# Kernel optimization log

Measured on AMD Instinct MI355X. Metric: run time of the kernel, lower is better.

Reference implementation:

```python
import jax, jax.numpy as jnp
import numpy as np

B, N, C, D = 8, 16384, 256, 32
EPS = 1e-6


def setup_inputs() -> dict:
    key = jax.random.key(0)
    ks = jax.random.split(key, 16)
    g = lambda k, shape, s=0.05: jax.random.normal(k, shape, dtype=jnp.float32) * s
    inp = {
        "x": g(ks[0], (B, N, C), 1.0),
        "y": g(ks[1], (B, N, C), 1.0),
        "Wq": g(ks[2], (D, C)), "bq": g(ks[3], (D,), 0.01),
        "Wk": g(ks[4], (D, C)), "bk": g(ks[5], (D,), 0.01),
        "Wv": g(ks[6], (C, C)), "bv": g(ks[7], (C,), 0.01),
        "Wqy": g(ks[8], (D, C)), "bqy": g(ks[9], (D,), 0.01),
        "Wky": g(ks[10], (D, C)), "bky": g(ks[11], (D,), 0.01),
        "Wvy": g(ks[12], (C, C)), "bvy": g(ks[13], (C,), 0.01),
        # gammas are nn.Parameter(torch.zeros(1)); random-init so outputs/grads are nontrivial
        "gamma": jnp.full((1,), 0.7, jnp.float32),
        "gamma_y": jnp.full((1,), 0.6, jnp.float32),
        "gamma_cx": jnp.full((1,), 0.5, jnp.float32),
        "gamma_cy": jnp.full((1,), 0.4, jnp.float32),
        "wx1": jnp.float32(0.5), "wx2": jnp.float32(0.5),
        "wy1": jnp.float32(0.5), "wy2": jnp.float32(0.5),
    }
    return inp


def _conv1x1(t, W, b):
    # t: [b,c,n]; 1x1 Conv2d == per-position linear
    return jnp.einsum('oc,bcn->bon', W, t) + b[None, :, None]


def _l2norm(t):
    # torch l2_norm: divide each spatial column by its channel-dim L2 norm
    return t / jnp.linalg.norm(t, axis=-2, keepdims=True)


def _branch(Qt, Ksum, mat, vsum, n):
    # Qt:[b,n,d]  Ksum:[b,d]  mat=K@V^T:[b,d,c]  vsum:[b,c]
    tailor = 1.0 / (n + jnp.einsum('bnd,bd->bn', Qt, Ksum))      # [b,n]
    msum = vsum[:, :, None] + jnp.einsum('bnd,bdc->bcn', Qt, mat)  # [b,c,n]
    return msum * tailor[:, None, :]


def reference(x, y, Wq, bq, Wk, bk, Wv, bv, Wqy, bqy, Wky, bky, Wvy, bvy,
              gamma, gamma_y, gamma_cx, gamma_cy, wx1, wx2, wy1, wy2):
    b, n, c = x.shape
    xb = jnp.transpose(x, (0, 2, 1))  # [b,c,n]
    yb = jnp.transpose(y, (0, 2, 1))
    Q = _l2norm(_conv1x1(xb, Wq, bq))      # [b,d,n]
    K = _l2norm(_conv1x1(xb, Wk, bk))
    V = _conv1x1(xb, Wv, bv)               # [b,c,n]
    Qy = _l2norm(_conv1x1(yb, Wqy, bqy))
    Ky = _l2norm(_conv1x1(yb, Wky, bky))
    Vy = _conv1x1(yb, Wvy, bvy)
    Qt = jnp.transpose(Q, (0, 2, 1))       # [b,n,d]
    Qyt = jnp.transpose(Qy, (0, 2, 1))
    Ksum = K.sum(-1) + EPS                 # [b,d]
    Kysum = Ky.sum(-1) + EPS
    vsum = V.sum(-1)                       # [b,c]
    vysum = Vy.sum(-1)
    mat = jnp.einsum('bdn,bcn->bdc', K, V)     # [b,d,c]
    maty = jnp.einsum('bdn,bcn->bdc', Ky, Vy)
    att = gamma * _branch(Qt, Ksum, mat, vsum, n)          # self x
    atty = gamma_y * _branch(Qyt, Kysum, maty, vysum, n)   # self y
    att_cx = gamma_cx * _branch(Qt, Kysum, maty, vsum, n)  # cross x<-y
    att_cy = gamma_cy * _branch(Qyt, Ksum, mat, vysum, n)  # cross y<-x
    fx = jnp.transpose(att * wx1 + att_cx * wx2, (0, 2, 1))  # [b,n,c]
    fy = jnp.transpose(atty * wy1 + att_cy * wy2, (0, 2, 1))
    return (fx, fy)
```

## Files before the change

kernel.cpp:

```cpp
#include <hip/hip_runtime.h>

#define BB 8
#define NN 16384
#define CC 256
#define DD 32
#define EPSF 1e-6f

#define QBUF_FLOATS (2ull*BB*NN*DD)
#define ACC_STRIDE 8480
#define ACC_OFF QBUF_FLOATS
#define ACC_FLOATS (16*ACC_STRIDE)
#define FIN_OFF (ACC_OFF + ACC_FLOATS)
#define FIN_STRIDE 8480
#define WBF_OFF (FIN_OFF + 16*FIN_STRIDE)

typedef __attribute__((ext_vector_type(8))) short bh8;
typedef __attribute__((ext_vector_type(4))) float f4;
typedef __attribute__((ext_vector_type(2))) unsigned int u32x2;

__device__ __forceinline__ unsigned int bfp(float f) {
    unsigned int u = __float_as_uint(f);
    return (u + 0x7FFFu + ((u >> 16) & 1u)) >> 16;
}
__device__ __forceinline__ float bf2f(unsigned int h) {
    return __uint_as_float(h << 16);
}

#define MFMA16 __builtin_amdgcn_mfma_f32_16x16x32_bf16

#define LBAR() do { \
    asm volatile("s_waitcnt lgkmcnt(0)" ::: "memory"); \
    __builtin_amdgcn_s_barrier(); \
    __builtin_amdgcn_sched_barrier(0); \
} while (0)

__global__ __launch_bounds__(256)
void k0_cvt(const float* __restrict__ Wk, const float* __restrict__ Wq,
            const float* __restrict__ Wky, const float* __restrict__ Wqy,
            unsigned short* __restrict__ wbf)
{
    int i = blockIdx.x * 256 + threadIdx.x;
    const float* p = (i < 8192) ? Wk : (i < 16384) ? Wq : (i < 24576) ? Wky : Wqy;
    wbf[i] = (unsigned short)bfp(p[i & 8191]);
}

__global__ __launch_bounds__(256, 3)
void k1_proj(const float* __restrict__ x, const float* __restrict__ y,
             const unsigned short* __restrict__ wbf,
             const float* __restrict__ bk, const float* __restrict__ bq,
             const float* __restrict__ bky, const float* __restrict__ bqy,
             unsigned short* __restrict__ qbuf16, float* __restrict__ acc,
             float* __restrict__ pbuf)
{
    const int b = blockIdx.y, s = blockIdx.z;
    const float* __restrict__ src = (s ? y : x) + (size_t)b * NN * CC;
    unsigned short* __restrict__ qb = qbuf16 + (size_t)(s*BB + b) * NN * DD;
    float* __restrict__ accsb = acc + (size_t)(s*BB + b) * ACC_STRIDE;
    float* __restrict__ pout = pbuf + ((size_t)((s*BB + b) * 64 + blockIdx.x)) * 8192;

    __shared__ unsigned short Xsub[2][8192];
    __shared__ unsigned short Ksb[1024];
    __shared__ float red[4][32];
    __shared__ float xred[4][256];

    const int tid = threadIdx.x;
    const int w = tid >> 6, lane = tid & 63;
    const int l15 = lane & 15, l4 = lane >> 4;
    const int oct = lane & 31;
    const int rower = tid >> 5;

    const unsigned short* __restrict__ wm =
        wbf + (size_t)(s * 2 + (w >> 1)) * 8192 + (size_t)(16 * (w & 1) + l15) * 256 + 8 * l4;
    bh8 wf[8];
    #pragma unroll
    for (int ks = 0; ks < 8; ++ks) wf[ks] = *(const bh8*)(wm + 32 * ks);
    const float* __restrict__ bp = (w < 2) ? (s ? bky : bk) : (s ? bqy : bq);
    const f4 bias4 = *(const f4*)(bp + 16 * (w & 1) + 4 * l4);

    const int hv = (rower >> 2) & 1;
    const int wbyte0 = (hv * 2048 + (oct >> 1) * 128 + (rower & 3) * 32 + (oct & 1) * 16) ^ (hv << 4);
    int ab[2];
    #pragma unroll
    for (int pt = 0; pt < 2; ++pt) {
        int aq = 4 * pt + (l15 >> 2);
        ab[pt] = ((aq * 2048 + (l15 & 3) * 32 + (l4 & 1) * 16) ^ ((aq & 1) << 4)) + (l4 >> 1) * 128;
    }
    const unsigned xb0 = (unsigned)(uintptr_t)&Xsub[0][0];
    const unsigned kbase = (unsigned)(uintptr_t)&Ksb[0];
    const unsigned btr_rel = (unsigned)(2 * l4 * 2048 + 4 * w * 128 + l15 * 8);
    const unsigned atr = kbase + (unsigned)(2 * l4 * 256 + l15 * 8);

    f4 g2[2][4];
    #pragma unroll
    for (int dt = 0; dt < 2; ++dt)
        #pragma unroll
        for (int ct = 0; ct < 4; ++ct) g2[dt][ct] = (f4){0.f, 0.f, 0.f, 0.f};
    float xs[8];
    #pragma unroll
    for (int j = 0; j < 8; ++j) xs[j] = 0.f;
    float kreg[4] = {0.f, 0.f, 0.f, 0.f};

    const float* __restrict__ gbase = src + (size_t)(blockIdx.x * 256 + rower) * CC + oct * 8;
    float4 va[4], vb[4];

    #pragma unroll
    for (int it = 0; it < 4; ++it) {
        const float* g = gbase + (size_t)(it * 8) * CC;
        va[it] = *(const float4*)g;
        vb[it] = *(const float4*)(g + 4);
    }

    for (int ch = 0; ch < 8; ++ch) {
        const int cur = ch & 1;
        char* xcur = (char*)&Xsub[cur][0];

        #pragma unroll
        for (int it = 0; it < 4; ++it) {
            float4 A = va[it], B = vb[it];
            xs[0] += A.x; xs[1] += A.y; xs[2] += A.z; xs[3] += A.w;
            xs[4] += B.x; xs[5] += B.y; xs[6] += B.z; xs[7] += B.w;
            uint4 pk;
            pk.x = bfp(A.x) | (bfp(A.y) << 16);
            pk.y = bfp(A.z) | (bfp(A.w) << 16);
            pk.z = bfp(B.x) | (bfp(B.y) << 16);
            pk.w = bfp(B.z) | (bfp(B.w) << 16);
            *(uint4*)(xcur + wbyte0 + it * 4096) = pk;
        }
        if (ch < 7) {
            const float* gn = gbase + (size_t)((ch + 1) * 32) * CC;
            #pragma unroll
            for (int it = 0; it < 4; ++it) {
                const float* g = gn + (size_t)(it * 8) * CC;
                va[it] = *(const float4*)g;
                vb[it] = *(const float4*)(g + 4);
            }
        }
        LBAR();

        f4 a1[2];
        #pragma unroll
        for (int pt = 0; pt < 2; ++pt) a1[pt] = bias4;
        #pragma unroll
        for (int ks = 0; ks < 8; ++ks) {
            #pragma unroll
            for (int pt = 0; pt < 2; ++pt) {
                bh8 xbv = *(const bh8*)(xcur + ab[pt] + ks * 256);
                a1[pt] = MFMA16(wf[ks], xbv, a1[pt], 0, 0, 0);
            }
        }

        #pragma unroll
        for (int pt = 0; pt < 2; ++pt) {
            float ssv = a1[pt][0]*a1[pt][0] + a1[pt][1]*a1[pt][1]
                      + a1[pt][2]*a1[pt][2] + a1[pt][3]*a1[pt][3];
            ssv += __shfl_xor(ssv, 16);
            ssv += __shfl_xor(ssv, 32);
            if (l4 == 0) red[w][16 * pt + l15] = ssv;
        }
        LBAR();

        if (w < 2) {
            #pragma unroll
            for (int pt = 0; pt < 2; ++pt) {
                int p = 16 * pt + l15;
                float n = rsqrtf(red[0][p] + red[1][p]);
                float k0 = a1[pt][0]*n, k1 = a1[pt][1]*n, k2 = a1[pt][2]*n, k3 = a1[pt][3]*n;
                kreg[0] += k0; kreg[1] += k1; kreg[2] += k2; kreg[3] += k3;
                unsigned lo = bfp(k0) | (bfp(k1) << 16);
                unsigned hi = bfp(k2) | (bfp(k3) << 16);
                *(uint2*)((char*)Ksb + (p >> 2) * 256 + (w & 1) * 128 + (p & 3) * 32 + 8 * l4)
                    = make_uint2(lo, hi);
            }
        } else {
            #pragma unroll
            for (int pt = 0; pt < 2; ++pt) {
                int p = 16 * pt + l15;
                float n = rsqrtf(red[2][p] + red[3][p]);
                unsigned lo = bfp(a1[pt][0]*n) | (bfp(a1[pt][1]*n) << 16);
                unsigned hi = bfp(a1[pt][2]*n) | (bfp(a1[pt][3]*n) << 16);
                *(uint2*)(qb + (size_t)(blockIdx.x*256 + ch*32 + p) * DD + 16 * (w & 1) + 4 * l4)
                    = make_uint2(lo, hi);
            }
        }
        LBAR();

        {
            const unsigned kb = xb0 + (unsigned)(cur * 16384) + btr_rel;
            u32x2 ta0, ta1, ta2, ta3, tb0, tb1, tb2, tb3, tb4, tb5, tb6, tb7;
            asm volatile("ds_read_b64_tr_b16 %0, %1" : "=v"(ta0) : "v"(atr));
            asm volatile("ds_read_b64_tr_b16 %0, %1" : "=v"(ta1) : "v"(atr + 256u));
            asm volatile("ds_read_b64_tr_b16 %0, %1" : "=v"(ta2) : "v"(atr + 128u));
            asm volatile("ds_read_b64_tr_b16 %0, %1" : "=v"(ta3) : "v"(atr + 384u));
            asm volatile("ds_read_b64_tr_b16 %0, %1" : "=v"(tb0) : "v"(kb));
            asm volatile("ds_read_b64_tr_b16 %0, %1" : "=v"(tb1) : "v"((kb + 2048u) ^ 16u));
            asm volatile("ds_read_b64_tr_b16 %0, %1" : "=v"(tb2) : "v"(kb + 128u));
            asm volatile("ds_read_b64_tr_b16 %0, %1" : "=v"(tb3) : "v"((kb + 2176u) ^ 16u));
            asm volatile("ds_read_b64_tr_b16 %0, %1" : "=v"(tb4) : "v"(kb + 256u));
            asm volatile("ds_read_b64_tr_b16 %0, %1" : "=v"(tb5) : "v"((kb + 2304u) ^ 16u));
            asm volatile("ds_read_b64_tr_b16 %0, %1" : "=v"(tb6) : "v"(kb + 384u));
            asm volatile("ds_read_b64_tr_b16 %0, %1" : "=v"(tb7) : "v"((kb + 2432u) ^ 16u));
            asm volatile("s_waitcnt lgkmcnt(8)" ::: "memory");
            __builtin_amdgcn_sched_barrier(0);
            union { unsigned u[4]; bh8 v; } A0, A1;
            A0.u[0] = ta0[0]; A0.u[1] = ta0[1]; A0.u[2] = ta1[0]; A0.u[3] = ta1[1];
            A1.u[0] = ta2[0]; A1.u[1] = ta2[1]; A1.u[2] = ta3[0]; A1.u[3] = ta3[1];
            asm volatile("s_waitcnt lgkmcnt(6)" ::: "memory");
            __builtin_amdgcn_sched_barrier(0);
            {
                union { unsigned u[4]; bh8 v; } Bc;
                Bc.u[0] = tb0[0]; Bc.u[1] = tb0[1]; Bc.u[2] = tb1[0]; Bc.u[3] = tb1[1];
                g2[0][0] = MFMA16(A0.v, Bc.v, g2[0][0], 0, 0, 0);
                g2[1][0] = MFMA16(A1.v, Bc.v, g2[1][0], 0, 0, 0);
            }
            asm volatile("s_waitcnt lgkmcnt(4)" ::: "memory");
            __builtin_amdgcn_sched_barrier(0);
            {
                union { unsigned u[4]; bh8 v; } Bc;
                Bc.u[0] = tb2[0]; Bc.u[1] = tb2[1]; Bc.u[2] = tb3[0]; Bc.u[3] = tb3[1];
                g2[0][1] = MFMA16(A0.v, Bc.v, g2[0][1], 0, 0, 0);
                g2[1][1] = MFMA16(A1.v, Bc.v, g2[1][1], 0, 0, 0);
            }
            asm volatile("s_waitcnt lgkmcnt(2)" ::: "memory");
            __builtin_amdgcn_sched_barrier(0);
            {
                union { unsigned u[4]; bh8 v; } Bc;
                Bc.u[0] = tb4[0]; Bc.u[1] = tb4[1]; Bc.u[2] = tb5[0]; Bc.u[3] = tb5[1];
                g2[0][2] = MFMA16(A0.v, Bc.v, g2[0][2], 0, 0, 0);
                g2[1][2] = MFMA16(A1.v, Bc.v, g2[1][2], 0, 0, 0);
            }
            asm volatile("s_waitcnt lgkmcnt(0)" ::: "memory");
            __builtin_amdgcn_sched_barrier(0);
            {
                union { unsigned u[4]; bh8 v; } Bc;
                Bc.u[0] = tb6[0]; Bc.u[1] = tb6[1]; Bc.u[2] = tb7[0]; Bc.u[3] = tb7[1];
                g2[0][3] = MFMA16(A0.v, Bc.v, g2[0][3], 0, 0, 0);
                g2[1][3] = MFMA16(A1.v, Bc.v, g2[1][3], 0, 0, 0);
            }
        }
    }

    #pragma unroll
    for (int dt = 0; dt < 2; ++dt)
        #pragma unroll
        for (int ct = 0; ct < 4; ++ct)
            #pragma unroll
            for (int r = 0; r < 4; ++r)
                pout[(16 * dt + 4 * l4 + r) * 256 + 64 * w + 16 * ct + l15] = g2[dt][ct][r];

    #pragma unroll
    for (int j = 0; j < 8; ++j) xs[j] += __shfl_xor(xs[j], 32);
    if ((lane >> 5) == 0) {
        #pragma unroll
        for (int j = 0; j < 8; ++j) xred[w][oct * 8 + j] = xs[j];
    }
    __syncthreads();
    {
        float v = xred[0][tid] + xred[1][tid] + xred[2][tid] + xred[3][tid];
        atomicAdd(accsb + 8192 + tid, v);
    }
    if (w < 2) {
        #pragma unroll
        for (int r = 0; r < 4; ++r) {
            float v = kreg[r];
            v += __shfl_xor(v, 1); v += __shfl_xor(v, 2);
            v += __shfl_xor(v, 4); v += __shfl_xor(v, 8);
            if (l15 == 0) atomicAdd(accsb + 8448 + 16 * (w & 1) + 4 * l4 + r, v);
        }
    }
}

__global__ __launch_bounds__(256)
void k2a_reduce(const float* __restrict__ pbuf, float* __restrict__ acc)
{
    const int b = blockIdx.x, s = blockIdx.y, cs = blockIdx.z;
    const float* __restrict__ p = pbuf + (size_t)(s*BB + b) * 64 * 8192;
    float* __restrict__ a = acc + (size_t)(s*BB + b) * ACC_STRIDE;
    const int d = threadIdx.x >> 3, c = cs * 32 + (threadIdx.x & 7) * 4;
    f4 v = (f4){0.f, 0.f, 0.f, 0.f};
    for (int j = 0; j < 64; ++j)
        v += *(const f4*)(p + (size_t)j * 8192 + d * 256 + c);
    *(f4*)(a + d * 256 + c) = v;
}

__global__ __launch_bounds__(256, 2)
void k2_finalize(const float* __restrict__ Wv, const float* __restrict__ bv,
                 const float* __restrict__ Wvy, const float* __restrict__ bvy,
                 const float* __restrict__ acc, float* __restrict__ fin)
{
    const int b = blockIdx.x, s = blockIdx.y;
    const float* __restrict__ Wv_ = s ? Wvy : Wv;
    const float* __restrict__ bv_ = s ? bvy : bv;
    const float* __restrict__ a = acc + (size_t)(s*BB + b) * ACC_STRIDE;
    float* __restrict__ f = fin + (size_t)(s*BB + b) * FIN_STRIDE;

    __shared__ float KXt[256][36];
    __shared__ float xsh[256];
    __shared__ float ks0[32];

    const int tid = threadIdx.x;
    for (int d = 0; d < 32; ++d) KXt[tid][d] = a[d*256 + tid];
    xsh[tid] = a[8192 + tid];
    if (tid < 32) { float v = a[8448 + tid]; ks0[tid] = v; f[8448 + tid] = v + EPSF; }
    __syncthreads();

    const int dh = tid >> 7;
    const int c0 = (tid & 127) * 2;
    float macc[16][2];
    #pragma unroll
    for (int i = 0; i < 16; ++i) { macc[i][0]=0.f; macc[i][1]=0.f; }
    float v0 = 0.f, v1 = 0.f;

    for (int k4 = 0; k4 < 256; k4 += 4) {
        float4 wa = *(const float4*)(Wv_ + (size_t)c0*256 + k4);
        float4 wb = *(const float4*)(Wv_ + (size_t)(c0+1)*256 + k4);
        float4 xv = *(const float4*)&xsh[k4];
        v0 += wa.x*xv.x + wa.y*xv.y + wa.z*xv.z + wa.w*xv.w;
        v1 += wb.x*xv.x + wb.y*xv.y + wb.z*xv.z + wb.w*xv.w;
        #pragma unroll
        for (int u = 0; u < 4; ++u) {
            float wau = (u==0)?wa.x:(u==1)?wa.y:(u==2)?wa.z:wa.w;
            float wbu = (u==0)?wb.x:(u==1)?wb.y:(u==2)?wb.z:wb.w;
            #pragma unroll
            for (int i4 = 0; i4 < 16; i4 += 4) {
                float4 kxv = *(const float4*)&KXt[k4+u][dh*16 + i4];
                macc[i4+0][0] += kxv.x*wau; macc[i4+0][1] += kxv.x*wbu;
                macc[i4+1][0] += kxv.y*wau; macc[i4+1][1] += kxv.y*wbu;
                macc[i4+2][0] += kxv.z*wau; macc[i4+2][1] += kxv.z*wbu;
                macc[i4+3][0] += kxv.w*wau; macc[i4+3][1] += kxv.w*wbu;
            }
        }
    }
    float bvc0 = bv_[c0], bvc1 = bv_[c0+1];
    if (dh == 0) {
        f[8192 + c0]     = v0 + (float)NN * bvc0;
        f[8192 + c0 + 1] = v1 + (float)NN * bvc1;
    }
    #pragma unroll
    for (int i = 0; i < 16; ++i) {
        int d = dh*16 + i;
        f[d*256 + c0]     = macc[i][0] + ks0[d]*bvc0;
        f[d*256 + c0 + 1] = macc[i][1] + ks0[d]*bvc1;
    }
}

__global__ __launch_bounds__(512, 2)
void k3_output(const unsigned short* __restrict__ qbuf16, const float* __restrict__ fin,
               const float* __restrict__ g_gamma, const float* __restrict__ g_gammay,
               const float* __restrict__ g_gammacx, const float* __restrict__ g_gammacy,
               const float* __restrict__ g_wx1, const float* __restrict__ g_wx2,
               const float* __restrict__ g_wy1, const float* __restrict__ g_wy2,
               float* __restrict__ out)
{
    const int b = blockIdx.y;
    const int p0 = blockIdx.x * 64;
    const float* __restrict__ fx_ = fin + (size_t)(0*BB + b) * FIN_STRIDE;
    const float* __restrict__ fy_ = fin + (size_t)(1*BB + b) * FIN_STRIDE;

    __shared__ unsigned short Msb[256 * 64];
    __shared__ unsigned short Atb[128 * 64];
    __shared__ float vs[2][256];
    __shared__ float sv[128];
    __shared__ float ksl[2][32];

    const int tid = threadIdx.x;

    if (tid < 64) ksl[tid >> 5][tid & 31] = ((tid < 32) ? fx_ : fy_)[8448 + (tid & 31)];
    vs[tid >> 8][tid & 255] = ((tid < 256) ? fx_ : fy_)[8192 + (tid & 255)];
    __syncthreads();

    #pragma unroll
    for (int i = 0; i < 4; ++i) {
        int task = tid * 4 + i;
        int c = task >> 3, kg = task & 7;
        const float* __restrict__ fp = ((kg < 4) ? fx_ : fy_) + (size_t)((kg & 3) * 8) * 256 + c;
        uint4 pk;
        pk.x = bfp(fp[0])    | (bfp(fp[256])  << 16);
        pk.y = bfp(fp[512])  | (bfp(fp[768])  << 16);
        pk.z = bfp(fp[1024]) | (bfp(fp[1280]) << 16);
        pk.w = bfp(fp[1536]) | (bfp(fp[1792]) << 16);
        unsigned off = (unsigned)(c * 128 + kg * 16) ^ (unsigned)((c & 7) << 4);
        *(uint4*)((char*)Msb + off) = pk;
    }

    if (tid < 128) {
        const int str = tid >> 6;
        const int p = p0 + (tid & 63);
        const uint4* __restrict__ qp = (const uint4*)(qbuf16 + ((size_t)(str*BB + b) * NN + p) * DD);
        float q[32];
        float ss = 0.f;
        #pragma unroll
        for (int m = 0; m < 4; ++m) {
            uint4 u = qp[m];
            unsigned uu[4] = {u.x, u.y, u.z, u.w};
            #pragma unroll
            for (int j = 0; j < 4; ++j) {
                float lo = bf2f(uu[j] & 0xFFFFu), hi = bf2f(uu[j] >> 16);
                q[m*8 + 2*j] = lo; q[m*8 + 2*j + 1] = hi;
                ss += lo*lo + hi*hi;
            }
        }
        float qn = rsqrtf(ss);
        float dK = 0.f, dKy = 0.f;
        #pragma unroll
        for (int d = 0; d < 32; ++d) { dK += q[d]*ksl[0][d]; dKy += q[d]*ksl[1][d]; }
        dK *= qn; dKy *= qn;
        float clo, chi, svr;
        if (str == 0) {
            float t1 = 1.f / ((float)NN + dK);
            float t2 = 1.f / ((float)NN + dKy);
            float a1c = g_gamma[0]   * g_wx1[0] * t1;
            float a2c = g_gammacx[0] * g_wx2[0] * t2;
            clo = a1c * qn; chi = a2c * qn; svr = a1c + a2c;
        } else {
            float ty1 = 1.f / ((float)NN + dKy);
            float ty2 = 1.f / ((float)NN + dK);
            float b1c = g_gammay[0]  * g_wy1[0] * ty1;
            float b2c = g_gammacy[0] * g_wy2[0] * ty2;
            clo = b2c * qn; chi = b1c * qn; svr = b1c + b2c;
        }
        sv[tid] = svr;
        #pragma unroll
        for (int g = 0; g < 8; ++g) {
            float m0 = (g < 4) ? clo : chi;
            const float* qq = q + (g & 3) * 8;
            uint4 pk;
            pk.x = bfp(m0*qq[0]) | (bfp(m0*qq[1]) << 16);
            pk.y = bfp(m0*qq[2]) | (bfp(m0*qq[3]) << 16);
            pk.z = bfp(m0*qq[4]) | (bfp(m0*qq[5]) << 16);
            pk.w = bfp(m0*qq[6]) | (bfp(m0*qq[7]) << 16);
            unsigned off = (unsigned)(tid * 128 + g * 16) ^ (unsigned)((tid & 7) << 4);
            *(uint4*)((char*)Atb + off) = pk;
        }
    }
    __syncthreads();

    const int w = tid >> 6, lane = tid & 63;
    const int l15 = lane & 15, l4 = lane >> 4;
    const int r = w * 16 + l15;
    f4 accv[16];
    #pragma unroll
    for (int ct = 0; ct < 16; ++ct) accv[ct] = (f4){0.f, 0.f, 0.f, 0.f};

    #pragma unroll
    for (int kstep = 0; kstep < 2; ++kstep) {
        unsigned boff = (unsigned)(r * 128 + kstep * 64 + l4 * 16) ^ (unsigned)((r & 7) << 4);
        bh8 bfr = *(const bh8*)((const char*)Atb + boff);
        #pragma unroll
        for (int ct = 0; ct < 16; ++ct) {
            int c = ct * 16 + l15;
            unsigned aoff = (unsigned)(c * 128 + kstep * 64 + l4 * 16) ^ (unsigned)((c & 7) << 4);
            bh8 afr = *(const bh8*)((const char*)Msb + aoff);
            accv[ct] = MFMA16(afr, bfr, accv[ct], 0, 0, 0);
        }
    }

    const int str = w >> 2;
    const int prow = (w & 3) * 16 + l15;
    float* __restrict__ op = out + (size_t)str * BB * NN * CC + ((size_t)b * NN + p0 + prow) * CC;
    const float svr = sv[r];
    #pragma unroll
    for (int ct = 0; ct < 16; ++ct) {
        int c0 = ct * 16 + 4 * l4;
        float4 vsv = *(const float4*)&vs[str][c0];
        float4 o = make_float4(accv[ct][0] + svr*vsv.x, accv[ct][1] + svr*vsv.y,
                               accv[ct][2] + svr*vsv.z, accv[ct][3] + svr*vsv.w);
        *(float4*)(op + c0) = o;
    }
}

extern "C" void kernel_launch(void* const* d_in, const int* in_sizes, int n_in,
                              void* d_out, int out_size, void* d_ws, size_t ws_size,
                              hipStream_t stream)
{
    (void)in_sizes; (void)n_in; (void)out_size; (void)ws_size;
    const float* x   = (const float*)d_in[0];
    const float* y   = (const float*)d_in[1];
    const float* Wq  = (const float*)d_in[2];
    const float* bq  = (const float*)d_in[3];
    const float* Wk  = (const float*)d_in[4];
    const float* bk  = (const float*)d_in[5];
    const float* Wv  = (const float*)d_in[6];
    const float* bv  = (const float*)d_in[7];
    const float* Wqy = (const float*)d_in[8];
    const float* bqy = (const float*)d_in[9];
    const float* Wky = (const float*)d_in[10];
    const float* bky = (const float*)d_in[11];
    const float* Wvy = (const float*)d_in[12];
    const float* bvy = (const float*)d_in[13];

    float* ws   = (float*)d_ws;
    unsigned short* qbuf16 = (unsigned short*)ws;
    float* acc  = ws + ACC_OFF;
    float* fin  = ws + FIN_OFF;
    unsigned short* wbf = (unsigned short*)(ws + WBF_OFF);
    float* pbuf = (float*)d_out;

    k0_cvt<<<128, 256, 0, stream>>>(Wk, Wq, Wky, Wqy, wbf);
    hipMemsetAsync(acc, 0, ACC_FLOATS * sizeof(float), stream);

    k1_proj<<<dim3(64, BB, 2), 256, 0, stream>>>(x, y, wbf, bk, bq, bky, bqy, qbuf16, acc, pbuf);
    k2a_reduce<<<dim3(BB, 2, 8), 256, 0, stream>>>(pbuf, acc);
    k2_finalize<<<dim3(BB, 2), 256, 0, stream>>>(Wv, bv, Wvy, bvy, acc, fin);
    k3_output<<<dim3(NN/64, BB), 512, 0, stream>>>(qbuf16, fin,
        (const float*)d_in[14], (const float*)d_in[15], (const float*)d_in[16], (const float*)d_in[17],
        (const float*)d_in[18], (const float*)d_in[19], (const float*)d_in[20], (const float*)d_in[21],
        (float*)d_out);
}
```

Measured before the change: 245.3 us.

## Precompute bf16 transposed mat in finalize; shrink output blocks; deepen projection prefetch

```diff
diff --git a/kernel.cpp b/kernel.cpp
--- a/kernel.cpp
+++ b/kernel.cpp
@@ -13,6 +13,7 @@
 #define FIN_OFF (ACC_OFF + ACC_FLOATS)
 #define FIN_STRIDE 8480
 #define WBF_OFF (FIN_OFF + 16*FIN_STRIDE)
+#define MATT_OFF (WBF_OFF + 16384)
 
 typedef __attribute__((ext_vector_type(8))) short bh8;
 typedef __attribute__((ext_vector_type(4))) float f4;
@@ -44,7 +45,7 @@
     wbf[i] = (unsigned short)bfp(p[i & 8191]);
 }
 
-__global__ __launch_bounds__(256, 3)
+__global__ __launch_bounds__(256, 4)
 void k1_proj(const float* __restrict__ x, const float* __restrict__ y,
              const unsigned short* __restrict__ wbf,
              const float* __restrict__ bk, const float* __restrict__ bq,
@@ -101,22 +102,25 @@
     float kreg[4] = {0.f, 0.f, 0.f, 0.f};
 
     const float* __restrict__ gbase = src + (size_t)(blockIdx.x * 256 + rower) * CC + oct * 8;
-    float4 va[4], vb[4];
-
-    #pragma unroll
-    for (int it = 0; it < 4; ++it) {
-        const float* g = gbase + (size_t)(it * 8) * CC;
-        va[it] = *(const float4*)g;
-        vb[it] = *(const float4*)(g + 4);
-    }
-
+    float4 va[2][4], vb[2][4];
+
+    #pragma unroll
+    for (int pc = 0; pc < 2; ++pc)
+        #pragma unroll
+        for (int it = 0; it < 4; ++it) {
+            const float* g = gbase + (size_t)(pc * 32 + it * 8) * CC;
+            va[pc][it] = *(const float4*)g;
+            vb[pc][it] = *(const float4*)(g + 4);
+        }
+
+    #pragma unroll 2
     for (int ch = 0; ch < 8; ++ch) {
         const int cur = ch & 1;
         char* xcur = (char*)&Xsub[cur][0];
 
         #pragma unroll
         for (int it = 0; it < 4; ++it) {
-            float4 A = va[it], B = vb[it];
+            float4 A = va[cur][it], B = vb[cur][it];
             xs[0] += A.x; xs[1] += A.y; xs[2] += A.z; xs[3] += A.w;
             xs[4] += B.x; xs[5] += B.y; xs[6] += B.z; xs[7] += B.w;
             uint4 pk;
@@ -126,13 +130,13 @@
             pk.w = bfp(B.z) | (bfp(B.w) << 16);
             *(uint4*)(xcur + wbyte0 + it * 4096) = pk;
         }
-        if (ch < 7) {
-            const float* gn = gbase + (size_t)((ch + 1) * 32) * CC;
+        if (ch < 6) {
+            const float* gn = gbase + (size_t)((ch + 2) * 32) * CC;
             #pragma unroll
             for (int it = 0; it < 4; ++it) {
                 const float* g = gn + (size_t)(it * 8) * CC;
-                va[it] = *(const float4*)g;
-                vb[it] = *(const float4*)(g + 4);
+                va[cur][it] = *(const float4*)g;
+                vb[cur][it] = *(const float4*)(g + 4);
             }
         }
         LBAR();
@@ -285,13 +289,15 @@
 __global__ __launch_bounds__(256, 2)
 void k2_finalize(const float* __restrict__ Wv, const float* __restrict__ bv,
                  const float* __restrict__ Wvy, const float* __restrict__ bvy,
-                 const float* __restrict__ acc, float* __restrict__ fin)
+                 const float* __restrict__ acc, float* __restrict__ fin,
+                 unsigned short* __restrict__ matT)
 {
     const int b = blockIdx.x, s = blockIdx.y;
     const float* __restrict__ Wv_ = s ? Wvy : Wv;
     const float* __restrict__ bv_ = s ? bvy : bv;
     const float* __restrict__ a = acc + (size_t)(s*BB + b) * ACC_STRIDE;
     float* __restrict__ f = fin + (size_t)(s*BB + b) * FIN_STRIDE;
+    unsigned short* __restrict__ mt = matT + (size_t)b * 16384;
 
     __shared__ float KXt[256][36];
     __shared__ float xsh[256];
@@ -335,16 +341,27 @@
         f[8192 + c0]     = v0 + (float)NN * bvc0;
         f[8192 + c0 + 1] = v1 + (float)NN * bvc1;
     }
+    union { unsigned short h[16]; uint4 q[2]; } r0u, r1u;
     #pragma unroll
     for (int i = 0; i < 16; ++i) {
         int d = dh*16 + i;
-        f[d*256 + c0]     = macc[i][0] + ks0[d]*bvc0;
-        f[d*256 + c0 + 1] = macc[i][1] + ks0[d]*bvc1;
-    }
-}
-
-__global__ __launch_bounds__(512, 2)
+        float m0v = macc[i][0] + ks0[d]*bvc0;
+        float m1v = macc[i][1] + ks0[d]*bvc1;
+        f[d*256 + c0]     = m0v;
+        f[d*256 + c0 + 1] = m1v;
+        r0u.h[i] = (unsigned short)bfp(m0v);
+        r1u.h[i] = (unsigned short)bfp(m1v);
+    }
+    const int kk = s * 32 + dh * 16;
+    *(uint4*)(mt + (size_t)c0 * 64 + kk)           = r0u.q[0];
+    *(uint4*)(mt + (size_t)c0 * 64 + kk + 8)       = r0u.q[1];
+    *(uint4*)(mt + (size_t)(c0+1) * 64 + kk)       = r1u.q[0];
+    *(uint4*)(mt + (size_t)(c0+1) * 64 + kk + 8)   = r1u.q[1];
+}
+
+__global__ __launch_bounds__(256, 4)
 void k3_output(const unsigned short* __restrict__ qbuf16, const float* __restrict__ fin,
+               const unsigned short* __restrict__ matT,
                const float* __restrict__ g_gamma, const float* __restrict__ g_gammay,
                const float* __restrict__ g_gammacx, const float* __restrict__ g_gammacy,
                const float* __restrict__ g_wx1, const float* __restrict__ g_wx2,
@@ -352,39 +369,24 @@
                float* __restrict__ out)
 {
     const int b = blockIdx.y;
-    const int p0 = blockIdx.x * 64;
+    const int p0 = blockIdx.x * 32;
     const float* __restrict__ fx_ = fin + (size_t)(0*BB + b) * FIN_STRIDE;
     const float* __restrict__ fy_ = fin + (size_t)(1*BB + b) * FIN_STRIDE;
 
-    __shared__ unsigned short Msb[256 * 64];
-    __shared__ unsigned short Atb[128 * 64];
+    __shared__ unsigned short Atb[64 * 64];
     __shared__ float vs[2][256];
-    __shared__ float sv[128];
+    __shared__ float sv[64];
     __shared__ float ksl[2][32];
 
     const int tid = threadIdx.x;
-
     if (tid < 64) ksl[tid >> 5][tid & 31] = ((tid < 32) ? fx_ : fy_)[8448 + (tid & 31)];
-    vs[tid >> 8][tid & 255] = ((tid < 256) ? fx_ : fy_)[8192 + (tid & 255)];
+    vs[0][tid] = fx_[8192 + tid];
+    vs[1][tid] = fy_[8192 + tid];
     __syncthreads();
 
-    #pragma unroll
-    for (int i = 0; i < 4; ++i) {
-        int task = tid * 4 + i;
-        int c = task >> 3, kg = task & 7;
-        const float* __restrict__ fp = ((kg < 4) ? fx_ : fy_) + (size_t)((kg & 3) * 8) * 256 + c;
-        uint4 pk;
-        pk.x = bfp(fp[0])    | (bfp(fp[256])  << 16);
-        pk.y = bfp(fp[512])  | (bfp(fp[768])  << 16);
-        pk.z = bfp(fp[1024]) | (bfp(fp[1280]) << 16);
-        pk.w = bfp(fp[1536]) | (bfp(fp[1792]) << 16);
-        unsigned off = (unsigned)(c * 128 + kg * 16) ^ (unsigned)((c & 7) << 4);
-        *(uint4*)((char*)Msb + off) = pk;
-    }
-
-    if (tid < 128) {
-        const int str = tid >> 6;
-        const int p = p0 + (tid & 63);
+    if (tid < 64) {
+        const int str = tid >> 5;
+        const int p = p0 + (tid & 31);
         const uint4* __restrict__ qp = (const uint4*)(qbuf16 + ((size_t)(str*BB + b) * NN + p) * DD);
         float q[32];
         float ss = 0.f;
@@ -437,6 +439,7 @@
     const int w = tid >> 6, lane = tid & 63;
     const int l15 = lane & 15, l4 = lane >> 4;
     const int r = w * 16 + l15;
+    const unsigned short* __restrict__ mb = matT + (size_t)b * 16384;
     f4 accv[16];
     #pragma unroll
     for (int ct = 0; ct < 16; ++ct) accv[ct] = (f4){0.f, 0.f, 0.f, 0.f};
@@ -447,15 +450,13 @@
         bh8 bfr = *(const bh8*)((const char*)Atb + boff);
         #pragma unroll
         for (int ct = 0; ct < 16; ++ct) {
-            int c = ct * 16 + l15;
-            unsigned aoff = (unsigned)(c * 128 + kstep * 64 + l4 * 16) ^ (unsigned)((c & 7) << 4);
-            bh8 afr = *(const bh8*)((const char*)Msb + aoff);
+            bh8 afr = *(const bh8*)(mb + (size_t)(ct * 16 + l15) * 64 + kstep * 32 + l4 * 8);
             accv[ct] = MFMA16(afr, bfr, accv[ct], 0, 0, 0);
         }
     }
 
-    const int str = w >> 2;
-    const int prow = (w & 3) * 16 + l15;
+    const int str = w >> 1;
+    const int prow = (w & 1) * 16 + l15;
     float* __restrict__ op = out + (size_t)str * BB * NN * CC + ((size_t)b * NN + p0 + prow) * CC;
     const float svr = sv[r];
     #pragma unroll
@@ -492,7 +493,8 @@
     unsigned short* qbuf16 = (unsigned short*)ws;
     float* acc  = ws + ACC_OFF;
     float* fin  = ws + FIN_OFF;
-    unsigned short* wbf = (unsigned short*)(ws + WBF_OFF);
+    unsigned short* wbf  = (unsigned short*)(ws + WBF_OFF);
+    unsigned short* matT = (unsigned short*)(ws + MATT_OFF);
     float* pbuf = (float*)d_out;
 
     k0_cvt<<<128, 256, 0, stream>>>(Wk, Wq, Wky, Wqy, wbf);
@@ -500,8 +502,8 @@
 
     k1_proj<<<dim3(64, BB, 2), 256, 0, stream>>>(x, y, wbf, bk, bq, bky, bqy, qbuf16, acc, pbuf);
     k2a_reduce<<<dim3(BB, 2, 8), 256, 0, stream>>>(pbuf, acc);
-    k2_finalize<<<dim3(BB, 2), 256, 0, stream>>>(Wv, bv, Wvy, bvy, acc, fin);
-    k3_output<<<dim3(NN/64, BB), 512, 0, stream>>>(qbuf16, fin,
+    k2_finalize<<<dim3(BB, 2), 256, 0, stream>>>(Wv, bv, Wvy, bvy, acc, fin, matT);
+    k3_output<<<dim3(NN/32, BB), 256, 0, stream>>>(qbuf16, fin, matT,
         (const float*)d_in[14], (const float*)d_in[15], (const float*)d_in[16], (const float*)d_in[17],
         (const float*)d_in[18], (const float*)d_in[19], (const float*)d_in[20], (const float*)d_in[21],
         (float*)d_out);
```

Result: slower. 408.6 us (+66.6%).
